# Kernel optimization log

Hardware: AMD Instinct MI355X
Metric: run time of the kernel (lower is better)

The kernel has to match this reference:

```python
import jax, jax.numpy as jnp
import numpy as np

ANGSTROM_TO_BOHR = 1.8897261258369282
CUTOFF = 5.2  # angstrom
N_SPECIES = 4  # H, C, N, O

# GFN1-xTB-style per-element constants for (H, C, N, O)
_ALPHA = np.array([2.209700, 1.247655, 1.524329, 1.845886], dtype=np.float32)
_Y_EFF = np.array([1.116244, 4.428763, 5.498808, 5.171786], dtype=np.float32)


def _smooth_cutoff(d, rc, eps=1e-10):
    # torchani 'smooth' cutoff: exp(1 - 1/(1 - (d/rc)^2)) for d < rc, else 0
    x2 = (d / rc) ** 2
    e = 1.0 - 1.0 / jnp.maximum(1.0 - x2, eps)
    return jnp.where(d < rc, jnp.exp(e), jnp.zeros_like(d))


def setup_inputs() -> dict:
    key = jax.random.key(0)
    k1, k2, k3 = jax.random.split(key, 3)
    M, A, P = 2048, 64, 8388608
    element_idxs = jax.random.randint(k1, (M, A), 0, N_SPECIES, dtype=jnp.int64)
    neighbor_idxs = jax.random.randint(k2, (2, P), 0, M * A, dtype=jnp.int64)
    distances = jax.random.uniform(k3, (P,), dtype=jnp.float32, minval=0.5, maxval=6.0)
    # precomputed pairwise parameter tables (buffers in the torch module)
    y_ab = jnp.asarray(np.outer(_Y_EFF, _Y_EFF))                 # [4,4]
    sqrt_alpha_ab = jnp.asarray(np.sqrt(np.outer(_ALPHA, _ALPHA)))  # [4,4]
    k_rep = np.full((N_SPECIES, N_SPECIES), 1.5, dtype=np.float32)
    k_rep[0, 0] = 1.0  # H-H
    k_rep_ab = jnp.asarray(k_rep)
    return {
        "element_idxs": element_idxs,
        "neighbor_idxs": neighbor_idxs,
        "distances": distances,
        "y_ab": y_ab,
        "sqrt_alpha_ab": sqrt_alpha_ab,
        "k_rep_ab": k_rep_ab,
    }


def reference(element_idxs, neighbor_idxs, distances, y_ab, sqrt_alpha_ab, k_rep_ab):
    M, A = element_idxs.shape
    d = jnp.clip(distances, 1e-7) * ANGSTROM_TO_BOHR  # [P] bohr
    species12 = element_idxs.reshape(-1)[neighbor_idxs]  # [2, P]
    s0, s1 = species12[0], species12[1]
    y = y_ab[s0, s1]                    # [P] gather
    sa = sqrt_alpha_ab[s0, s1]          # [P]
    kr = k_rep_ab[s0, s1]               # [P]
    rep = (y / d) * jnp.exp(-sa * d ** kr)
    rep = rep * _smooth_cutoff(d, CUTOFF * ANGSTROM_TO_BOHR)
    mol_idx = neighbor_idxs[0] // A     # [P]
    energies = jax.ops.segment_sum(rep, mol_idx, num_segments=M)  # [M]
    return energies
```

## Files before the change

### kernel.cpp

```cpp
#include <hip/hip_runtime.h>


#define AB_D 1.8897261258369282
#define L2E  1.4426950408889634f

__global__ __launch_bounds__(256) void pack_zero_kernel(
    const int* __restrict__ elem, int natoms, int nwords,
    unsigned* __restrict__ packed, float* __restrict__ out, int M)
{
    int g = blockIdx.x * blockDim.x + threadIdx.x;
    if (g < M) out[g] = 0.0f;
    if (g < nwords) {
        int base = g * 16;
        unsigned w = 0u;
        if (base + 16 <= natoms) {
            const int4* p = (const int4*)(elem + base);
            #pragma unroll
            for (int q = 0; q < 4; ++q) {
                int4 v = p[q];
                w |= ((unsigned)v.x & 3u) << (2 * (4 * q + 0));
                w |= ((unsigned)v.y & 3u) << (2 * (4 * q + 1));
                w |= ((unsigned)v.z & 3u) << (2 * (4 * q + 2));
                w |= ((unsigned)v.w & 3u) << (2 * (4 * q + 3));
            }
        } else {
            for (int j = 0; j < 16; ++j) {
                int a = base + j;
                unsigned s = (a < natoms) ? ((unsigned)elem[a] & 3u) : 0u;
                w |= s << (2 * j);
            }
        }
        packed[g] = w;
    }
}

__device__ __forceinline__ float sel4(unsigned s, float a, float b, float c, float d)
{
    float lo = (s & 1u) ? b : a;
    float hi = (s & 1u) ? d : c;
    return (s & 2u) ? hi : lo;
}

__global__ __launch_bounds__(1024, 8) void rep_main_kernel(
    const int* __restrict__ nbr, const float* __restrict__ dist,
    const unsigned* __restrict__ packed_g,
    const float* __restrict__ y_ab, const float* __restrict__ sa_ab,
    long long P, int M, int nwords, int ashift, int A,
    unsigned cmask, int use_swz,
    float* __restrict__ partials, float* __restrict__ out, int mode)
{
    extern __shared__ char smem[];
    float*    acc = (float*)smem;
    unsigned* pk  = (unsigned*)(smem + (size_t)M * 4);

    const int tid  = threadIdx.x;
    const int nthr = blockDim.x;

    for (int m = tid; m < M; m += nthr) acc[m] = 0.0f;
    for (int w = tid; w < nwords; w += nthr) pk[w] = packed_g[w];

    const float yv0 = sqrtf(y_ab[0]),  yv1 = sqrtf(y_ab[5]);
    const float yv2 = sqrtf(y_ab[10]), yv3 = sqrtf(y_ab[15]);
    const float sL2E = sqrtf(L2E);
    const float av0 = sqrtf(sa_ab[0])  * sL2E, av1 = sqrtf(sa_ab[5])  * sL2E;
    const float av2 = sqrtf(sa_ab[10]) * sL2E, av3 = sqrtf(sa_ab[15]) * sL2E;
    __syncthreads();

    const float ABf   = (float)AB_D;
    const float DMIN  = (float)(1e-7 * AB_D);
    const float RC    = (float)(5.2 * AB_D);
    const float RCINV = (float)(1.0 / (5.2 * AB_D));
    const int* nb0 = nbr;
    const int* nb1 = nbr + P;

    auto process_one = [&](unsigned ua0, unsigned ua1, float draw) {
        unsigned s0 = (pk[ua0 >> 4] >> ((ua0 & 15u) * 2u)) & 3u;
        unsigned s1 = (pk[ua1 >> 4] >> ((ua1 & 15u) * 2u)) & 3u;
        float y  = sel4(s0, yv0, yv1, yv2, yv3) * sel4(s1, yv0, yv1, yv2, yv3);
        float sa = sel4(s0, av0, av1, av2, av3) * sel4(s1, av0, av1, av2, av3);
        float d    = fmaxf(draw * ABf, DMIN);
        float sq   = __builtin_amdgcn_sqrtf(d);
        float fac  = ((s0 | s1) == 0u) ? 1.0f : sq;
        float drep = d * fac;
        float x    = d * RCINV;
        float om   = fmaf(-x, x, 1.0f);
        float r    = __builtin_amdgcn_rcpf(om);
        float e    = fmaf(-L2E, r, L2E);
        float arg  = fmaf(-sa, drep, e);
        float rep  = y * __builtin_amdgcn_rcpf(d) * __builtin_amdgcn_exp2f(arg);
        rep = (d < RC) ? rep : 0.0f;
        unsigned mol = (ashift >= 0) ? (ua0 >> ashift) : (ua0 / (unsigned)A);
        atomicAdd(&acc[mol], rep);
    };

    auto process_quad = [&](int4 i0, int4 i1, float4 dv) {
        unsigned a0[4] = {(unsigned)i0.x, (unsigned)i0.y, (unsigned)i0.z, (unsigned)i0.w};
        unsigned a1[4] = {(unsigned)i1.x, (unsigned)i1.y, (unsigned)i1.z, (unsigned)i1.w};
        float    dr[4] = {dv.x, dv.y, dv.z, dv.w};
        unsigned w0[4], w1[4];
        #pragma unroll
        for (int j = 0; j < 4; ++j) {
            w0[j] = pk[a0[j] >> 4];
            w1[j] = pk[a1[j] >> 4];
        }
        #pragma unroll
        for (int j = 0; j < 4; ++j) {
            unsigned s0 = (w0[j] >> ((a0[j] & 15u) * 2u)) & 3u;
            unsigned s1 = (w1[j] >> ((a1[j] & 15u) * 2u)) & 3u;
            float y  = sel4(s0, yv0, yv1, yv2, yv3) * sel4(s1, yv0, yv1, yv2, yv3);
            float sa = sel4(s0, av0, av1, av2, av3) * sel4(s1, av0, av1, av2, av3);
            float d    = fmaxf(dr[j] * ABf, DMIN);
            float sq   = __builtin_amdgcn_sqrtf(d);
            float fac  = ((s0 | s1) == 0u) ? 1.0f : sq;
            float drep = d * fac;
            float x    = d * RCINV;
            float om   = fmaf(-x, x, 1.0f);
            float r    = __builtin_amdgcn_rcpf(om);
            float e    = fmaf(-L2E, r, L2E);
            float arg  = fmaf(-sa, drep, e);
            float rep  = y * __builtin_amdgcn_rcpf(d) * __builtin_amdgcn_exp2f(arg);
            rep = (d < RC) ? rep : 0.0f;
            unsigned mol = (ashift >= 0) ? (a0[j] >> ashift) : (a0[j] / (unsigned)A);
            atomicAdd(&acc[mol], rep);
        }
    };

    const int  lane = tid & 63;
    long long P4 = P >> 2;
    long long C  = P4 >> 6;
    long long W  = ((long long)gridDim.x * nthr) >> 6;
    long long wg = (((long long)blockIdx.x * nthr + tid)) >> 6;

    auto swz = [&](long long c) -> long long {
        if (!use_swz) return c;
        return (long long)(((unsigned)c * 2654435761u) & cmask);
    };
    auto load3 = [&](long long c, int4& i0, int4& i1, float4& dv) {
        long long q = (c << 6) + lane;
        i0 = ((const int4*)nb0)[q];
        i1 = ((const int4*)nb1)[q];
        dv = ((const float4*)dist)[q];
    };

    for (long long c = wg; c < C; c += 2 * W) {
        long long cB = c + W;
        bool hasB = (cB < C);
        int4 A0, A1, B0, B1; float4 D0, D1;
        load3(swz(c), A0, A1, D0);
        if (hasB) load3(swz(cB), B0, B1, D1);
        process_quad(A0, A1, D0);
        if (hasB) process_quad(B0, B1, D1);
    }

    if (blockIdx.x == 0) {
        for (long long q = (C << 6) + tid; q < P4; q += nthr) {
            int4   i0 = ((const int4*)nb0)[q];
            int4   i1 = ((const int4*)nb1)[q];
            float4 dv = ((const float4*)dist)[q];
            process_quad(i0, i1, dv);
        }
        for (long long p = (P4 << 2) + tid; p < P; p += nthr)
            process_one((unsigned)nb0[p], (unsigned)nb1[p], dist[p]);
    }
    __syncthreads();

    if (mode == 0) {
        float* row = partials + (size_t)blockIdx.x * (size_t)M;
        for (int m = tid; m < M; m += nthr) row[m] = acc[m];
    } else {
        for (int m = tid; m < M; m += nthr) {
            float v = acc[m];
            if (v != 0.0f) atomicAdd(&out[m], v);
        }
    }
}

__global__ __launch_bounds__(256) void reduce_kernel(
    const float* __restrict__ partials, float* __restrict__ out,
    int M, int nblk, int rows_per)
{
    int m = blockIdx.x * blockDim.x + threadIdx.x;
    if (m >= M) return;
    int r0 = blockIdx.y * rows_per;
    int r1 = r0 + rows_per;
    if (r1 > nblk) r1 = nblk;
    if (r0 >= r1) return;
    float s0 = 0.f, s1 = 0.f, s2 = 0.f, s3 = 0.f;
    int r = r0;
    for (; r + 3 < r1; r += 4) {
        s0 += partials[(size_t)(r + 0) * M + m];
        s1 += partials[(size_t)(r + 1) * M + m];
        s2 += partials[(size_t)(r + 2) * M + m];
        s3 += partials[(size_t)(r + 3) * M + m];
    }
    for (; r < r1; ++r) s0 += partials[(size_t)r * M + m];
    atomicAdd(&out[m], (s0 + s1) + (s2 + s3));
}

extern "C" void kernel_launch(void* const* d_in, const int* in_sizes, int n_in,
                              void* d_out, int out_size, void* d_ws, size_t ws_size,
                              hipStream_t stream)
{
    const int*   elem  = (const int*)d_in[0];
    const int*   nbr   = (const int*)d_in[1];
    const float* dist  = (const float*)d_in[2];
    const float* y_ab  = (const float*)d_in[3];
    const float* sa_ab = (const float*)d_in[4];
    float* out = (float*)d_out;

    const int natoms = in_sizes[0];
    const long long P = (long long)in_sizes[2];
    const int M = out_size;
    const int A = natoms / M;
    int ashift = -1;
    if (A > 0 && (A & (A - 1)) == 0) {
        int s = 0;
        while ((1 << s) < A) ++s;
        ashift = s;
    }
    const int nwords = (natoms + 15) / 16;

    long long P4 = P >> 2;
    long long C  = P4 >> 6;
    int use_swz = (C > 1 && (C & (C - 1)) == 0) ? 1 : 0;
    unsigned cmask = use_swz ? (unsigned)(C - 1) : 0u;

    size_t packed_bytes = ((size_t)nwords * 4 + 255) & ~(size_t)255;
    if (ws_size < packed_bytes) return;
    unsigned* packed = (unsigned*)d_ws;

    const int BLOCK = 1024;
    int nblk = 512;
    float* partials = nullptr;
    int mode = 1;
    {
        size_t avail = ws_size - packed_bytes;
        size_t rowb = (size_t)M * 4;
        long long maxrows = (long long)(avail / rowb);
        if (maxrows >= 64) {
            nblk = (int)(maxrows < 512 ? maxrows : 512);
            partials = (float*)((char*)d_ws + packed_bytes);
            mode = 0;
        }
    }

    {
        int total = (nwords > M) ? nwords : M;
        int g = (total + 255) / 256;
        hipLaunchKernelGGL(pack_zero_kernel, dim3(g), dim3(256), 0, stream,
                           elem, natoms, nwords, packed, out, M);
    }

    {
        size_t smem = (size_t)M * 4 + (size_t)nwords * 4;
        hipLaunchKernelGGL(rep_main_kernel, dim3(nblk), dim3(BLOCK), smem, stream,
                           nbr, dist, packed, y_ab, sa_ab,
                           P, M, nwords, ashift, A, cmask, use_swz,
                           partials, out, mode);
    }

    if (mode == 0) {
        const int SPLIT = 32;
        int rows_per = (nblk + SPLIT - 1) / SPLIT;
        dim3 grid((M + 255) / 256, SPLIT);
        hipLaunchKernelGGL(reduce_kernel, grid, dim3(256), 0, stream,
                           partials, out, M, nblk, rows_per);
    }
}
```

Measured before the change: 158.6 us.

## Double-buffer pair streams into LDS with async global_load_lds pipeline

Replaces the register-load grid-stride main loop with a block-contiguous chunked loop. Twelve waves asynchronously copy 4 KB chunks of each of the two index streams and the distance stream into a double-buffered LDS staging area via global_load_lds, waiting with s_waitcnt and block barriers. Each thread then processes one pair per chunk. Pairs beyond the cutoff now skip the species lookup, the math and the atomic entirely. The aim is to overlap global streaming with compute and to cut wasted work, at the cost of two block barriers per chunk, a fixed 64 KB LDS footprint that limits occupancy, and a separate fallback kernel for shapes outside the fast path.

```diff
diff --git a/kernel.cpp b/kernel.cpp
--- a/kernel.cpp
+++ b/kernel.cpp
@@ -4,29 +4,31 @@
 #define AB_D 1.8897261258369282
 #define L2E  1.4426950408889634f
 
+typedef unsigned int u32;
+
 __global__ __launch_bounds__(256) void pack_zero_kernel(
     const int* __restrict__ elem, int natoms, int nwords,
-    unsigned* __restrict__ packed, float* __restrict__ out, int M)
+    u32* __restrict__ packed, float* __restrict__ out, int M)
 {
     int g = blockIdx.x * blockDim.x + threadIdx.x;
     if (g < M) out[g] = 0.0f;
     if (g < nwords) {
         int base = g * 16;
-        unsigned w = 0u;
+        u32 w = 0u;
         if (base + 16 <= natoms) {
             const int4* p = (const int4*)(elem + base);
             #pragma unroll
             for (int q = 0; q < 4; ++q) {
                 int4 v = p[q];
-                w |= ((unsigned)v.x & 3u) << (2 * (4 * q + 0));
-                w |= ((unsigned)v.y & 3u) << (2 * (4 * q + 1));
-                w |= ((unsigned)v.z & 3u) << (2 * (4 * q + 2));
-                w |= ((unsigned)v.w & 3u) << (2 * (4 * q + 3));
+                w |= ((u32)v.x & 3u) << (2 * (4 * q + 0));
+                w |= ((u32)v.y & 3u) << (2 * (4 * q + 1));
+                w |= ((u32)v.z & 3u) << (2 * (4 * q + 2));
+                w |= ((u32)v.w & 3u) << (2 * (4 * q + 3));
             }
         } else {
             for (int j = 0; j < 16; ++j) {
                 int a = base + j;
-                unsigned s = (a < natoms) ? ((unsigned)elem[a] & 3u) : 0u;
+                u32 s = (a < natoms) ? ((u32)elem[a] & 3u) : 0u;
                 w |= s << (2 * j);
             }
         }
@@ -34,30 +36,40 @@
     }
 }
 
-__device__ __forceinline__ float sel4(unsigned s, float a, float b, float c, float d)
+__device__ __forceinline__ float sel4(u32 s, float a, float b, float c, float d)
 {
     float lo = (s & 1u) ? b : a;
     float hi = (s & 1u) ? d : c;
     return (s & 2u) ? hi : lo;
 }
 
-__global__ __launch_bounds__(1024, 8) void rep_main_kernel(
+__device__ __forceinline__ void async_load16(const void* g, void* lds_base)
+{
+    __builtin_amdgcn_global_load_lds(
+        (const __attribute__((address_space(1))) u32*)g,
+        (__attribute__((address_space(3))) u32*)lds_base,
+        16, 0, 0);
+}
+
+__global__ __launch_bounds__(1024, 8) void rep_pipe_kernel(
     const int* __restrict__ nbr, const float* __restrict__ dist,
-    const unsigned* __restrict__ packed_g,
+    const u32* __restrict__ packed_g,
     const float* __restrict__ y_ab, const float* __restrict__ sa_ab,
-    long long P, int M, int nwords, int ashift, int A,
-    unsigned cmask, int use_swz,
-    float* __restrict__ partials, float* __restrict__ out, int mode)
-{
-    extern __shared__ char smem[];
-    float*    acc = (float*)smem;
-    unsigned* pk  = (unsigned*)(smem + (size_t)M * 4);
+    long long P, int M, int nwords, int ashift,
+    int chunks_per_block, long long total_chunks,
+    float* __restrict__ partials)
+{
+    __shared__ char smem[65536];
+    float* acc   = (float*)smem;
+    u32*   pk    = (u32*)(smem + 8192);
+    char*  stage = smem + 40960;
 
     const int tid  = threadIdx.x;
-    const int nthr = blockDim.x;
-
-    for (int m = tid; m < M; m += nthr) acc[m] = 0.0f;
-    for (int w = tid; w < nwords; w += nthr) pk[w] = packed_g[w];
+    const int wave = tid >> 6;
+    const int lane = tid & 63;
+
+    for (int m = tid; m < M; m += 1024) acc[m] = 0.0f;
+    for (int w = tid; w < nwords; w += 1024) pk[w] = packed_g[w];
 
     const float yv0 = sqrtf(y_ab[0]),  yv1 = sqrtf(y_ab[5]);
     const float yv2 = sqrtf(y_ab[10]), yv3 = sqrtf(y_ab[15]);
@@ -70,46 +82,37 @@
     const float DMIN  = (float)(1e-7 * AB_D);
     const float RC    = (float)(5.2 * AB_D);
     const float RCINV = (float)(1.0 / (5.2 * AB_D));
-    const int* nb0 = nbr;
-    const int* nb1 = nbr + P;
-
-    auto process_one = [&](unsigned ua0, unsigned ua1, float draw) {
-        unsigned s0 = (pk[ua0 >> 4] >> ((ua0 & 15u) * 2u)) & 3u;
-        unsigned s1 = (pk[ua1 >> 4] >> ((ua1 & 15u) * 2u)) & 3u;
-        float y  = sel4(s0, yv0, yv1, yv2, yv3) * sel4(s1, yv0, yv1, yv2, yv3);
-        float sa = sel4(s0, av0, av1, av2, av3) * sel4(s1, av0, av1, av2, av3);
-        float d    = fmaxf(draw * ABf, DMIN);
-        float sq   = __builtin_amdgcn_sqrtf(d);
-        float fac  = ((s0 | s1) == 0u) ? 1.0f : sq;
-        float drep = d * fac;
-        float x    = d * RCINV;
-        float om   = fmaf(-x, x, 1.0f);
-        float r    = __builtin_amdgcn_rcpf(om);
-        float e    = fmaf(-L2E, r, L2E);
-        float arg  = fmaf(-sa, drep, e);
-        float rep  = y * __builtin_amdgcn_rcpf(d) * __builtin_amdgcn_exp2f(arg);
-        rep = (d < RC) ? rep : 0.0f;
-        unsigned mol = (ashift >= 0) ? (ua0 >> ashift) : (ua0 / (unsigned)A);
-        atomicAdd(&acc[mol], rep);
+
+    const char* g_nb0  = (const char*)nbr;
+    const char* g_nb1  = (const char*)(nbr + P);
+    const char* g_dist = (const char*)dist;
+
+    const long long c0 = (long long)blockIdx.x * chunks_per_block;
+
+    auto stage_load = [&](int buf, long long c) {
+        if (wave < 12 && c < total_chunks) {
+            int stream = wave >> 2, seg = wave & 3;
+            const char* gb = (stream == 0) ? g_nb0 : (stream == 1) ? g_nb1 : g_dist;
+            const char* gp = gb + (c << 12) + (seg << 10) + ((long long)lane << 4);
+            char* lp = stage + buf * 12288 + stream * 4096 + seg * 1024;
+            async_load16(gp, lp);
+        }
     };
 
-    auto process_quad = [&](int4 i0, int4 i1, float4 dv) {
-        unsigned a0[4] = {(unsigned)i0.x, (unsigned)i0.y, (unsigned)i0.z, (unsigned)i0.w};
-        unsigned a1[4] = {(unsigned)i1.x, (unsigned)i1.y, (unsigned)i1.z, (unsigned)i1.w};
-        float    dr[4] = {dv.x, dv.y, dv.z, dv.w};
-        unsigned w0[4], w1[4];
-        #pragma unroll
-        for (int j = 0; j < 4; ++j) {
-            w0[j] = pk[a0[j] >> 4];
-            w1[j] = pk[a1[j] >> 4];
-        }
-        #pragma unroll
-        for (int j = 0; j < 4; ++j) {
-            unsigned s0 = (w0[j] >> ((a0[j] & 15u) * 2u)) & 3u;
-            unsigned s1 = (w1[j] >> ((a1[j] & 15u) * 2u)) & 3u;
+    auto process_chunk = [&](int buf, long long c) {
+        if (c >= total_chunks) return;
+        const u32*   b0 = (const u32*)(stage + buf * 12288);
+        const u32*   b1 = (const u32*)(stage + buf * 12288 + 4096);
+        const float* bd = (const float*)(stage + buf * 12288 + 8192);
+        u32   ua0  = b0[tid];
+        u32   ua1  = b1[tid];
+        float draw = bd[tid];
+        float d = fmaxf(draw * ABf, DMIN);
+        if (d < RC) {
+            u32 s0 = (pk[ua0 >> 4] >> ((ua0 & 15u) * 2u)) & 3u;
+            u32 s1 = (pk[ua1 >> 4] >> ((ua1 & 15u) * 2u)) & 3u;
             float y  = sel4(s0, yv0, yv1, yv2, yv3) * sel4(s1, yv0, yv1, yv2, yv3);
             float sa = sel4(s0, av0, av1, av2, av3) * sel4(s1, av0, av1, av2, av3);
-            float d    = fmaxf(dr[j] * ABf, DMIN);
             float sq   = __builtin_amdgcn_sqrtf(d);
             float fac  = ((s0 | s1) == 0u) ? 1.0f : sq;
             float drep = d * fac;
@@ -119,59 +122,96 @@
             float e    = fmaf(-L2E, r, L2E);
             float arg  = fmaf(-sa, drep, e);
             float rep  = y * __builtin_amdgcn_rcpf(d) * __builtin_amdgcn_exp2f(arg);
-            rep = (d < RC) ? rep : 0.0f;
-            unsigned mol = (ashift >= 0) ? (a0[j] >> ashift) : (a0[j] / (unsigned)A);
+            atomicAdd(&acc[ua0 >> ashift], rep);
+        }
+    };
+
+    stage_load(0, c0);
+    const int nc = chunks_per_block;
+    for (int i = 0; i + 1 < nc; ++i) {
+        stage_load((i + 1) & 1, c0 + i + 1);
+        asm volatile("s_waitcnt vmcnt(1)" ::: "memory");
+        __builtin_amdgcn_s_barrier();
+        process_chunk(i & 1, c0 + i);
+        __builtin_amdgcn_s_barrier();
+    }
+    asm volatile("s_waitcnt vmcnt(0)" ::: "memory");
+    __builtin_amdgcn_s_barrier();
+    process_chunk((nc - 1) & 1, c0 + nc - 1);
+
+    __syncthreads();
+    float* row = partials + (size_t)blockIdx.x * (size_t)M;
+    for (int m = tid; m < M; m += 1024) row[m] = acc[m];
+}
+
+__global__ __launch_bounds__(1024, 8) void rep_fallback_kernel(
+    const int* __restrict__ nbr, const float* __restrict__ dist,
+    const u32* __restrict__ packed_g,
+    const float* __restrict__ y_ab, const float* __restrict__ sa_ab,
+    long long P, int M, int nwords, int ashift, int A,
+    float* __restrict__ out)
+{
+    extern __shared__ char smem[];
+    float* acc = (float*)smem;
+    u32*   pk  = (u32*)(smem + (size_t)M * 4);
+
+    const int tid = threadIdx.x, nthr = blockDim.x;
+    for (int m = tid; m < M; m += nthr) acc[m] = 0.0f;
+    for (int w = tid; w < nwords; w += nthr) pk[w] = packed_g[w];
+    const float yv0 = sqrtf(y_ab[0]),  yv1 = sqrtf(y_ab[5]);
+    const float yv2 = sqrtf(y_ab[10]), yv3 = sqrtf(y_ab[15]);
+    const float sL2E = sqrtf(L2E);
+    const float av0 = sqrtf(sa_ab[0])  * sL2E, av1 = sqrtf(sa_ab[5])  * sL2E;
+    const float av2 = sqrtf(sa_ab[10]) * sL2E, av3 = sqrtf(sa_ab[15]) * sL2E;
+    __syncthreads();
+
+    const float ABf   = (float)AB_D;
+    const float DMIN  = (float)(1e-7 * AB_D);
+    const float RC    = (float)(5.2 * AB_D);
+    const float RCINV = (float)(1.0 / (5.2 * AB_D));
+
+    auto process = [&](u32 ua0, u32 ua1, float draw) {
+        float d = fmaxf(draw * ABf, DMIN);
+        if (d < RC) {
+            u32 s0 = (pk[ua0 >> 4] >> ((ua0 & 15u) * 2u)) & 3u;
+            u32 s1 = (pk[ua1 >> 4] >> ((ua1 & 15u) * 2u)) & 3u;
+            float y  = sel4(s0, yv0, yv1, yv2, yv3) * sel4(s1, yv0, yv1, yv2, yv3);
+            float sa = sel4(s0, av0, av1, av2, av3) * sel4(s1, av0, av1, av2, av3);
+            float sq   = __builtin_amdgcn_sqrtf(d);
+            float fac  = ((s0 | s1) == 0u) ? 1.0f : sq;
+            float drep = d * fac;
+            float x    = d * RCINV;
+            float om   = fmaf(-x, x, 1.0f);
+            float r    = __builtin_amdgcn_rcpf(om);
+            float e    = fmaf(-L2E, r, L2E);
+            float arg  = fmaf(-sa, drep, e);
+            float rep  = y * __builtin_amdgcn_rcpf(d) * __builtin_amdgcn_exp2f(arg);
+            u32 mol = (ashift >= 0) ? (ua0 >> ashift) : (ua0 / (u32)A);
             atomicAdd(&acc[mol], rep);
         }
     };
 
-    const int  lane = tid & 63;
     long long P4 = P >> 2;
-    long long C  = P4 >> 6;
-    long long W  = ((long long)gridDim.x * nthr) >> 6;
-    long long wg = (((long long)blockIdx.x * nthr + tid)) >> 6;
-
-    auto swz = [&](long long c) -> long long {
-        if (!use_swz) return c;
-        return (long long)(((unsigned)c * 2654435761u) & cmask);
-    };
-    auto load3 = [&](long long c, int4& i0, int4& i1, float4& dv) {
-        long long q = (c << 6) + lane;
-        i0 = ((const int4*)nb0)[q];
-        i1 = ((const int4*)nb1)[q];
-        dv = ((const float4*)dist)[q];
-    };
-
-    for (long long c = wg; c < C; c += 2 * W) {
-        long long cB = c + W;
-        bool hasB = (cB < C);
-        int4 A0, A1, B0, B1; float4 D0, D1;
-        load3(swz(c), A0, A1, D0);
-        if (hasB) load3(swz(cB), B0, B1, D1);
-        process_quad(A0, A1, D0);
-        if (hasB) process_quad(B0, B1, D1);
-    }
-
+    long long gstride = (long long)gridDim.x * nthr;
+    const int* nb0 = nbr;
+    const int* nb1 = nbr + P;
+    for (long long q = (long long)blockIdx.x * nthr + tid; q < P4; q += gstride) {
+        int4   i0 = ((const int4*)nb0)[q];
+        int4   i1 = ((const int4*)nb1)[q];
+        float4 dv = ((const float4*)dist)[q];
+        process((u32)i0.x, (u32)i1.x, dv.x);
+        process((u32)i0.y, (u32)i1.y, dv.y);
+        process((u32)i0.z, (u32)i1.z, dv.z);
+        process((u32)i0.w, (u32)i1.w, dv.w);
+    }
     if (blockIdx.x == 0) {
-        for (long long q = (C << 6) + tid; q < P4; q += nthr) {
-            int4   i0 = ((const int4*)nb0)[q];
-            int4   i1 = ((const int4*)nb1)[q];
-            float4 dv = ((const float4*)dist)[q];
-            process_quad(i0, i1, dv);
-        }
         for (long long p = (P4 << 2) + tid; p < P; p += nthr)
-            process_one((unsigned)nb0[p], (unsigned)nb1[p], dist[p]);
-    }
-    __syncthreads();
-
-    if (mode == 0) {
-        float* row = partials + (size_t)blockIdx.x * (size_t)M;
-        for (int m = tid; m < M; m += nthr) row[m] = acc[m];
-    } else {
-        for (int m = tid; m < M; m += nthr) {
-            float v = acc[m];
-            if (v != 0.0f) atomicAdd(&out[m], v);
-        }
+            process((u32)nb0[p], (u32)nb1[p], dist[p]);
+    }
+    __syncthreads();
+    for (int m = tid; m < M; m += nthr) {
+        float v = acc[m];
+        if (v != 0.0f) atomicAdd(&out[m], v);
     }
 }
 
@@ -211,7 +251,7 @@
     const int natoms = in_sizes[0];
     const long long P = (long long)in_sizes[2];
     const int M = out_size;
-    const int A = natoms / M;
+    const int A = (M > 0) ? natoms / M : 1;
     int ashift = -1;
     if (A > 0 && (A & (A - 1)) == 0) {
         int s = 0;
@@ -220,29 +260,16 @@
     }
     const int nwords = (natoms + 15) / 16;
 
-    long long P4 = P >> 2;
-    long long C  = P4 >> 6;
-    int use_swz = (C > 1 && (C & (C - 1)) == 0) ? 1 : 0;
-    unsigned cmask = use_swz ? (unsigned)(C - 1) : 0u;
-
     size_t packed_bytes = ((size_t)nwords * 4 + 255) & ~(size_t)255;
-    if (ws_size < packed_bytes) return;
-    unsigned* packed = (unsigned*)d_ws;
-
-    const int BLOCK = 1024;
-    int nblk = 512;
-    float* partials = nullptr;
-    int mode = 1;
-    {
-        size_t avail = ws_size - packed_bytes;
-        size_t rowb = (size_t)M * 4;
-        long long maxrows = (long long)(avail / rowb);
-        if (maxrows >= 64) {
-            nblk = (int)(maxrows < 512 ? maxrows : 512);
-            partials = (float*)((char*)d_ws + packed_bytes);
-            mode = 0;
-        }
-    }
+    if (ws_size < (size_t)nwords * 4) return;
+    u32* packed = (u32*)d_ws;
+
+    const int NBLK = 512;
+    bool have_partials = (ws_size >= packed_bytes + (size_t)NBLK * M * 4);
+    float* partials = have_partials ? (float*)((char*)d_ws + packed_bytes) : nullptr;
+
+    bool fast = have_partials && (ashift >= 0) && (M >= 1) && (M <= 2048) &&
+                (nwords <= 8192) && (P > 0) && (P % 1024 == 0);
 
     {
         int total = (nwords > M) ? nwords : M;
@@ -251,19 +278,21 @@
                            elem, natoms, nwords, packed, out, M);
     }
 
-    {
-        size_t smem = (size_t)M * 4 + (size_t)nwords * 4;
-        hipLaunchKernelGGL(rep_main_kernel, dim3(nblk), dim3(BLOCK), smem, stream,
+    if (fast) {
+        long long total_chunks = P / 1024;
+        int cpb = (int)((total_chunks + NBLK - 1) / NBLK);
+        hipLaunchKernelGGL(rep_pipe_kernel, dim3(NBLK), dim3(1024), 0, stream,
                            nbr, dist, packed, y_ab, sa_ab,
-                           P, M, nwords, ashift, A, cmask, use_swz,
-                           partials, out, mode);
-    }
-
-    if (mode == 0) {
+                           P, M, nwords, ashift, cpb, total_chunks, partials);
         const int SPLIT = 32;
-        int rows_per = (nblk + SPLIT - 1) / SPLIT;
+        int rows_per = (NBLK + SPLIT - 1) / SPLIT;
         dim3 grid((M + 255) / 256, SPLIT);
         hipLaunchKernelGGL(reduce_kernel, grid, dim3(256), 0, stream,
-                           partials, out, M, nblk, rows_per);
-    }
-}
+                           partials, out, M, NBLK, rows_per);
+    } else {
+        size_t smem = (size_t)M * 4 + (size_t)nwords * 4;
+        hipLaunchKernelGGL(rep_fallback_kernel, dim3(NBLK), dim3(1024), smem, stream,
+                           nbr, dist, packed, y_ab, sa_ab,
+                           P, M, nwords, ashift, A, out);
+    }
+}
```

Measured after the change: 202.3 us. 27.5% more time.
